# Performance work log

Hardware: AMD Instinct MI355X
Metric: run time of the kernel (lower is better)

Reference implementation:

```python
import jax, jax.numpy as jnp
import numpy as np

K = 3
BN_EPS = 1e-3


def setup_inputs() -> dict:
    key = jax.random.key(0)
    ks = jax.random.split(key, 13)
    B, N1, N2 = 8, 1024, 4096
    C1, C2, Cs = 256, 128, 64
    Ctot = C1 + C2 + Cs  # 448
    H = 256
    return {
        "points1": jax.random.normal(ks[0], (B, 3, N1), jnp.float32),
        "points2": jax.random.normal(ks[1], (B, 3, N2), jnp.float32),
        "features1": jax.random.normal(ks[2], (B, C1, N1), jnp.float32),
        "features2": jax.random.normal(ks[3], (B, C2, N2), jnp.float32),
        "skip_features": jax.random.normal(ks[4], (B, Cs, N2), jnp.float32),
        # 1x1 Conv2d weights are equivalent to dense matrices [out, in]
        "W1": jax.random.normal(ks[5], (H, Ctot), jnp.float32) * 0.05,
        "b1": jax.random.normal(ks[6], (H,), jnp.float32) * 0.05,
        "g1": 1.0 + jax.random.normal(ks[7], (H,), jnp.float32) * 0.05,
        "beta1": jax.random.normal(ks[8], (H,), jnp.float32) * 0.05,
        "W2": jax.random.normal(ks[9], (H, H), jnp.float32) * 0.05,
        "b2": jax.random.normal(ks[10], (H,), jnp.float32) * 0.05,
        "g2": 1.0 + jax.random.normal(ks[11], (H,), jnp.float32) * 0.05,
        "beta2": jax.random.normal(ks[12], (H,), jnp.float32) * 0.05,
    }


def _conv_bn_relu(x, W, b, g, beta):
    # x: [B, N, Cin]; 1x1 conv == dense matmul per point
    y = jnp.einsum("bnc,oc->bno", x, W) + b
    # BatchNorm2d in training mode: batch stats over (batch, spatial) per channel
    mu = jnp.mean(y, axis=(0, 1))
    var = jnp.mean(jnp.square(y - mu), axis=(0, 1))  # biased variance
    y = (y - mu) * jax.lax.rsqrt(var + BN_EPS) * g + beta
    return jax.nn.relu(y)


def reference(points1, points2, features1, features2, skip_features,
              W1, b1, g1, beta1, W2, b2, g2, beta2):
    p1 = jnp.swapaxes(points1, 1, 2)  # [B, N1, 3]
    p2 = jnp.swapaxes(points2, 1, 2)  # [B, N2, 3]
    # pairwise Euclidean distances [B, N2, N1]
    d2 = (jnp.sum(p2 * p2, -1, keepdims=True)
          + jnp.sum(p1 * p1, -1)[:, None, :]
          - 2.0 * jnp.einsum("bnd,bmd->bnm", p2, p1))
    dist = jnp.sqrt(jnp.maximum(d2, 0.0))
    # k smallest distances
    neg_top, ind = jax.lax.top_k(-dist, K)  # ind: [B, N2, K]
    dk = -neg_top
    inv = 1.0 / (dk + 1e-10)
    w = inv / jnp.sum(inv, -1, keepdims=True)  # [B, N2, K]
    f1 = jnp.swapaxes(features1, 1, 2)  # [B, N1, C1]
    gathered = jax.vmap(lambda f, i: f[i])(f1, ind)  # [B, N2, K, C1]
    new = jnp.einsum("bnkc,bnk->bnc", gathered, w)  # inverse-distance interp
    x = jnp.concatenate([new,
                         jnp.swapaxes(features2, 1, 2),
                         jnp.swapaxes(skip_features, 1, 2)], axis=-1)
    x = _conv_bn_relu(x, W1, b1, g1, beta1)
    x = _conv_bn_relu(x, W2, b2, g2, beta2)
    return jnp.swapaxes(x, 1, 2)  # [B, Cout, N2]
```

## Files before the change

### kernel.cpp

```cpp
#include <hip/hip_runtime.h>
#include <cstdint>
#include <cstddef>

#define B_    8
#define N1_   1024
#define N2_   4096
#define C1_   256
#define C2_   128
#define CS_   64
#define CT_   448
#define H_    256
#define ROWS_ (B_ * N2_)
#define XW_   192

typedef __attribute__((ext_vector_type(8))) short bf16x8;
typedef __attribute__((ext_vector_type(4))) float f32x4;
typedef unsigned short ushort_t;
typedef unsigned int   uint_t;

__device__ __forceinline__ ushort_t f2bf(float f) {
    uint_t u = __float_as_uint(f);
    u = (u + 0x7fffu + ((u >> 16) & 1u)) >> 16;
    return (ushort_t)u;
}
__device__ __forceinline__ float bf2f(ushort_t h) {
    return __uint_as_float(((uint_t)h) << 16);
}
__device__ __forceinline__ void glds16(const void* g, void* l) {
    __builtin_amdgcn_global_load_lds(
        (const __attribute__((address_space(1))) void*)g,
        (__attribute__((address_space(3))) void*)l, 16, 0, 0);
}

__device__ __forceinline__ void tile_decode(int d, int& m0, int& n0) {
    const int j = d >> 3;
    m0 = ((d & 7) * 32 + (j >> 2)) * 128;
    n0 = (j & 3) * 64;
}

__global__ __launch_bounds__(256) void fused_pre(
    const float* __restrict__ p1, const float* __restrict__ p2,
    int* __restrict__ ind, float* __restrict__ wout,
    const float* __restrict__ f1, const float* __restrict__ f2,
    const float* __restrict__ fs, const float* __restrict__ W1,
    const float* __restrict__ W2, ushort_t* __restrict__ f1t,
    ushort_t* __restrict__ x, ushort_t* __restrict__ W1b, ushort_t* __restrict__ W2b)
{
#pragma clang fp contract(off)
    __shared__ __align__(16) char smem[32000];
    const int t = threadIdx.x;
    const int bid = blockIdx.x;
    if (bid < 1024) {
        float4*   cand  = (float4*)(smem);
        float*    pvals = (float*)(smem + 16512);
        float*    thr   = (float*)(smem + 19584);
        ushort_t* lists = (ushort_t*)(smem + 19712);
        float*    pdd   = (float*)(smem + 25856);
        int*      pdi   = (int*)(smem + 28928);
        const int b  = bid >> 7;
        const int qb = (bid & 127) * 32;
        const float* pb1 = p1 + (size_t)b * 3 * N1_;
        for (int i = t; i < N1_; i += 256) {
            float X = pb1[i], Y = pb1[N1_ + i], Z = pb1[2 * N1_ + i];
            cand[i] = make_float4(X, Y, Z, (X * X + Y * Y) + Z * Z);
        }
        const int q = t & 31, split = t >> 5;
        const int n = qb + q;
        const float* pb2 = p2 + (size_t)b * 3 * N2_;
        const float ax = pb2[n], ay = pb2[N2_ + n], az = pb2[2 * N2_ + n];
        const float s2a = (ax * ax + ay * ay) + az * az;
        const float m2x = -2.0f * ax, m2y = -2.0f * ay, m2z = -2.0f * az;
        __syncthreads();
        const int ibeg = split * 128, iend = ibeg + 128;
        {
            float a0 = 3e38f, a1 = 3e38f, a2 = 3e38f;
            for (int i = ibeg; i < iend; ++i) {
                float4 c = cand[i];
                float fd = fmaf(c.x, m2x, fmaf(c.y, m2y, fmaf(c.z, m2z, s2a + c.w)));
                float o0 = a0, o1 = a1;
                a0 = fminf(o0, fd);
                a1 = __builtin_amdgcn_fmed3f(fd, o0, o1);
                a2 = __builtin_amdgcn_fmed3f(fd, o1, a2);
            }
            pvals[t * 3 + 0] = a0; pvals[t * 3 + 1] = a1; pvals[t * 3 + 2] = a2;
        }
        __syncthreads();
        if (t < 32) {
            float m0 = 3e38f, m1 = 3e38f, m2v = 3e38f;
#pragma unroll
            for (int g = 0; g < 8; ++g)
#pragma unroll
                for (int r = 0; r < 3; ++r) {
                    float v = pvals[(g * 32 + t) * 3 + r];
                    float o0 = m0, o1 = m1;
                    m0 = fminf(o0, v);
                    m1 = __builtin_amdgcn_fmed3f(v, o0, o1);
                    m2v = __builtin_amdgcn_fmed3f(v, o1, m2v);
                }
            thr[t] = m2v + 2e-3f;
        }
        __syncthreads();
        const float th = thr[q];
        ushort_t* mylist = lists + (q * 8 + split) * 12;
        int cnt = 0;
        for (int i = ibeg; i < iend; ++i) {
            float4 c = cand[i];
            float fd = fmaf(c.x, m2x, fmaf(c.y, m2y, fmaf(c.z, m2z, s2a + c.w)));
            if (fd <= th && cnt < 12) { mylist[cnt] = (ushort_t)i; cnt++; }
        }
        float e0 = 3e38f, e1 = 3e38f, e2 = 3e38f;
        int   j0 = 0, j1 = 0, j2 = 0;
        for (int k = 0; k < cnt; ++k) {
            const int i = mylist[k];
            float4 c = cand[i];
            float dot = (ax * c.x + ay * c.y) + az * c.z;
            float dd  = (s2a + c.w) - 2.0f * dot;
            float d   = sqrtf(fmaxf(dd, 0.0f));
            if (d < e0)      { e2 = e1; j2 = j1; e1 = e0; j1 = j0; e0 = d; j0 = i; }
            else if (d < e1) { e2 = e1; j2 = j1; e1 = d;  j1 = i; }
            else if (d < e2) { e2 = d;  j2 = i; }
        }
        pdd[(split * 32 + q) * 3 + 0] = e0; pdi[(split * 32 + q) * 3 + 0] = j0;
        pdd[(split * 32 + q) * 3 + 1] = e1; pdi[(split * 32 + q) * 3 + 1] = j1;
        pdd[(split * 32 + q) * 3 + 2] = e2; pdi[(split * 32 + q) * 3 + 2] = j2;
        __syncthreads();
        if (t < 32) {
            float f0 = 3e38f, f1v = 3e38f, f2v = 3e38f;
            int   k0 = 0, k1 = 0, k2 = 0;
#pragma unroll
            for (int g = 0; g < 8; ++g)
#pragma unroll
                for (int r = 0; r < 3; ++r) {
                    float d = pdd[(g * 32 + t) * 3 + r];
                    int   i = pdi[(g * 32 + t) * 3 + r];
                    if (d < f0)       { f2v = f1v; k2 = k1; f1v = f0; k1 = k0; f0 = d; k0 = i; }
                    else if (d < f1v) { f2v = f1v; k2 = k1; f1v = d;  k1 = i; }
                    else if (d < f2v) { f2v = d;  k2 = i; }
                }
            float inv0 = 1.0f / (f0 + 1e-10f);
            float inv1 = 1.0f / (f1v + 1e-10f);
            float inv2 = 1.0f / (f2v + 1e-10f);
            float s = (inv0 + inv1) + inv2;
            const size_t row = (size_t)b * N2_ + qb + t;
            wout[row * 3 + 0] = inv0 / s;
            wout[row * 3 + 1] = inv1 / s;
            wout[row * 3 + 2] = inv2 / s;
            ind[row * 3 + 0] = k0;
            ind[row * 3 + 1] = k1;
            ind[row * 3 + 2] = k2;
        }
    } else if (bid < 1536) {
        float (*tile)[65] = (float (*)[65])smem;
        const int bid2 = bid - 1024;
        const int b  = bid2 >> 6;
        const int ct = (bid2 >> 4) & 3;
        const int nt = bid2 & 15;
        const int c0 = ct * 64, n0 = nt * 64;
        const float* src = f1 + ((size_t)b * C1_ + c0) * N1_ + n0;
#pragma unroll
        for (int j = 0; j < 16; ++j) {
            int lin = j * 256 + t;
            int ci = lin >> 6, nj = lin & 63;
            tile[ci][nj] = src[(size_t)ci * N1_ + nj];
        }
        __syncthreads();
        ushort_t* dst = f1t + ((size_t)b * N1_ + n0) * C1_ + c0;
#pragma unroll
        for (int j = 0; j < 8; ++j) {
            int lin = j * 256 + t;
            int ni = lin >> 5, cjp = (lin & 31) * 2;
            uint_t u = (uint_t)f2bf(tile[cjp][ni]) | ((uint_t)f2bf(tile[cjp + 1][ni]) << 16);
            *(uint_t*)&dst[(size_t)ni * C1_ + cjp] = u;
        }
    } else if (bid < 3072) {
        float (*tile)[65] = (float (*)[65])smem;
        const int bid2 = bid - 1536;
        const int b   = bid2 / 192;
        const int rem = bid2 - b * 192;
        const int ct  = rem >> 6;
        const int nt  = rem & 63;
        const float* src;
        if (ct < 2) src = f2 + ((size_t)b * C2_ + ct * 64) * N2_;
        else        src = fs + (size_t)b * CS_ * N2_;
        const int coff = ct * 64;
        const int n0 = nt * 64;
#pragma unroll
        for (int j = 0; j < 16; ++j) {
            int lin = j * 256 + t;
            int ci = lin >> 6, nj = lin & 63;
            tile[ci][nj] = src[(size_t)ci * N2_ + n0 + nj];
        }
        __syncthreads();
#pragma unroll
        for (int j = 0; j < 8; ++j) {
            int lin = j * 256 + t;
            int ni = lin >> 5, cjp = (lin & 31) * 2;
            uint_t u = (uint_t)f2bf(tile[cjp][ni]) | ((uint_t)f2bf(tile[cjp + 1][ni]) << 16);
            *(uint_t*)&x[((size_t)b * N2_ + n0 + ni) * XW_ + coff + cjp] = u;
        }
    } else {
        const int i = (bid - 3072) * 256 + t;
        if (i < H_ * CT_) W1b[i] = f2bf(W1[i]);
        if (i < H_ * H_)  W2b[i] = f2bf(W2[i]);
    }
}

__global__ __launch_bounds__(512, 6) void gemm1_fused(
    const ushort_t* __restrict__ f1t, const int* __restrict__ ind,
    const float* __restrict__ wgt, const ushort_t* __restrict__ x2,
    const ushort_t* __restrict__ Bw, const float* __restrict__ bias,
    ushort_t* __restrict__ C, float* __restrict__ ssum, float* __restrict__ ssq)
{
    __shared__ __align__(16) ushort_t smem[20480];
    ushort_t* As = smem;
    ushort_t* Bs = smem + 4096;
    ushort_t* Cs = smem;
    const int t = threadIdx.x;
    const int m0 = blockIdx.x * 64;
    const int lane = t & 63;
    const int wv = t >> 6;
    const int wr = wv & 1;
    const int wc = wv >> 1;
    const int lm = lane & 15, lq = lane >> 4;
    const int lrow8  = lane >> 3;
    const int lchunk = (lane & 7) ^ lrow8;
    const int aswz = lm & 7;
    const ushort_t* gB = Bw + (size_t)(wv * 32 + lrow8) * CT_ + lchunk * 8;
    ushort_t* lB = Bs + wv * 2048;
    const ushort_t* gA = x2 + (size_t)(m0 + wv * 8 + lrow8) * XW_ + lchunk * 8;
    ushort_t* lA = As + wv * 512;
    const int arow = t >> 3;
    const int ac0  = t & 7;
    const size_t grow = (size_t)m0 + arow;
    const int bb_ = (int)(grow >> 12);
    const int* ip = ind + grow * 3;
    const float* wp = wgt + grow * 3;
    const ushort_t* fb = f1t + (size_t)bb_ * N1_ * C1_;
    const ushort_t* ga0 = fb + (size_t)ip[0] * C1_ + ac0 * 8;
    const ushort_t* ga1 = fb + (size_t)ip[1] * C1_ + ac0 * 8;
    const ushort_t* ga2 = fb + (size_t)ip[2] * C1_ + ac0 * 8;
    const float w0 = wp[0], w1 = wp[1], w2 = wp[2];
    ushort_t* awr = As + arow * 64;
    const int arsw = arow & 7;
    f32x4 acc[2][4];
#pragma unroll
    for (int i = 0; i < 2; ++i)
#pragma unroll
        for (int j = 0; j < 4; ++j)
            acc[i][j] = (f32x4){0.f, 0.f, 0.f, 0.f};

    for (int k0 = 0; k0 < CT_; k0 += 64) {
        __syncthreads();
        if (k0 < 256) {
            uint4 va = *(const uint4*)(ga0 + k0);
            uint4 vb = *(const uint4*)(ga1 + k0);
            uint4 vc = *(const uint4*)(ga2 + k0);
            const uint_t* pa = (const uint_t*)&va;
            const uint_t* pb = (const uint_t*)&vb;
            const uint_t* pc = (const uint_t*)&vc;
            uint_t o[4];
#pragma unroll
            for (int e = 0; e < 4; ++e) {
                float lo = w0 * bf2f((ushort_t)(pa[e] & 0xffff))
                         + w1 * bf2f((ushort_t)(pb[e] & 0xffff))
                         + w2 * bf2f((ushort_t)(pc[e] & 0xffff));
                float hi = w0 * bf2f((ushort_t)(pa[e] >> 16))
                         + w1 * bf2f((ushort_t)(pb[e] >> 16))
                         + w2 * bf2f((ushort_t)(pc[e] >> 16));
                o[e] = (uint_t)f2bf(lo) | ((uint_t)f2bf(hi) << 16);
            }
            *(uint4*)&awr[(ac0 ^ arsw) * 8] = *(uint4*)o;
        } else {
            glds16(gA + (k0 - 256), lA);
        }
#pragma unroll
        for (int g = 0; g < 4; ++g)
            glds16(gB + k0 + g * 8 * CT_, lB + g * 512);
        __syncthreads();
#pragma unroll
        for (int h = 0; h < 2; ++h) {
            bf16x8 af[2], bfr[4];
#pragma unroll
            for (int i = 0; i < 2; ++i)
                af[i] = *(const bf16x8*)&As[(wr * 32 + i * 16 + lm) * 64
                                            + (((h * 4 + lq) ^ aswz)) * 8];
#pragma unroll
            for (int j = 0; j < 4; ++j)
                bfr[j] = *(const bf16x8*)&Bs[(wc * 64 + j * 16 + lm) * 64
                                             + (((h * 4 + lq) ^ aswz)) * 8];
#pragma unroll
            for (int i = 0; i < 2; ++i)
#pragma unroll
                for (int j = 0; j < 4; ++j)
                    acc[i][j] = __builtin_amdgcn_mfma_f32_16x16x32_bf16(af[i], bfr[j], acc[i][j], 0, 0, 0);
        }
    }
    __syncthreads();
#pragma unroll
    for (int j = 0; j < 4; ++j) {
        const int gn = wc * 64 + j * 16 + lm;
        const float bb = bias[gn];
        float ps = 0.0f, pq = 0.0f;
#pragma unroll
        for (int i = 0; i < 2; ++i) {
            const int row_l = wr * 32 + i * 16 + lq * 4;
            f32x4 v = acc[i][j];
#pragma unroll
            for (int r = 0; r < 4; ++r) {
                float val = v[r] + bb;
                ps += val;
                pq += val * val;
                float vo = __shfl_xor(val, 1);
                uint_t packed = (lm & 1)
                    ? ((uint_t)f2bf(vo)  | ((uint_t)f2bf(val) << 16))
                    : ((uint_t)f2bf(val) | ((uint_t)f2bf(vo)  << 16));
                if ((lm & 1) == 0)
                    *(uint_t*)&Cs[(row_l + r) * 264 + (gn & ~1)] = packed;
            }
        }
        ps += __shfl_xor(ps, 16); pq += __shfl_xor(pq, 16);
        ps += __shfl_xor(ps, 32); pq += __shfl_xor(pq, 32);
        if (lane < 16) {
            atomicAdd(&ssum[gn], ps);
            atomicAdd(&ssq[gn], pq);
        }
    }
    __syncthreads();
    const int srow = t >> 5;
    const int scol = (t & 31) * 8;
#pragma unroll
    for (int rep = 0; rep < 4; ++rep) {
        const int row = srow + rep * 16;
        uint4 v = *(const uint4*)&Cs[row * 264 + scol];
        *(uint4*)(C + (size_t)(m0 + row) * H_ + scol) = v;
    }
}

__global__ __launch_bounds__(256, 4) void gemm2_fused(
    const ushort_t* __restrict__ A, const ushort_t* __restrict__ Bw,
    const float* __restrict__ bias,
    const float* __restrict__ s1, const float* __restrict__ q1,
    const float* __restrict__ g1, const float* __restrict__ be1,
    ushort_t* __restrict__ C, float* __restrict__ ssum, float* __restrict__ ssq)
{
    __shared__ __align__(16) ushort_t smem[15360];
    ushort_t* As0 = smem;
    ushort_t* As1 = smem + 5120;
    ushort_t* Bs  = smem + 10240;
    float*    sc  = (float*)(smem + 14336);
    float*    sh  = (float*)(smem + 14848);
    ushort_t* Cs  = smem;
    const int t = threadIdx.x;
    int m0, n0;
    tile_decode(blockIdx.x, m0, n0);
    const int lane = t & 63;
    const int wv = t >> 6;
    const int wrow = wv & 1, wcol = wv >> 1;
    const int lm = lane & 15, lq = lane >> 4;
    const int lrow8  = lane >> 3;
    const int lchunk = (lane & 7) ^ lrow8;
    const int aswz = lm & 7;
    const int arow = t >> 1, acol = (t & 1) * 32;
    {
        const float invN = 1.0f / (float)ROWS_;
        float mu  = s1[t] * invN;
        float var = q1[t] * invN - mu * mu;
        float s   = rsqrtf(var + 1e-3f) * g1[t];
        sc[t] = s;
        sh[t] = be1[t] - mu * s;
    }
    const ushort_t* gB = Bw + (size_t)(n0 + wv * 16 + lrow8) * H_ + lchunk * 8;
    ushort_t* lB = Bs + wv * 1024;
    const ushort_t* gA = A + (size_t)(m0 + arow) * H_ + acol;
    ushort_t* As_t = (t & 1) ? As1 : As0;
    f32x4 acc[4][2];
#pragma unroll
    for (int i = 0; i < 4; ++i)
#pragma unroll
        for (int j = 0; j < 2; ++j)
            acc[i][j] = (f32x4){0.f, 0.f, 0.f, 0.f};

    for (int k0 = 0; k0 < H_; k0 += 64) {
        uint4 av[4];
#pragma unroll
        for (int g = 0; g < 4; ++g)
            av[g] = *(const uint4*)(gA + k0 + g * 8);
        __syncthreads();
#pragma unroll
        for (int g = 0; g < 2; ++g)
            glds16(gB + k0 + g * 8 * H_, lB + g * 512);
#pragma unroll
        for (int g = 0; g < 4; ++g) {
            const uint_t* wsrc = (const uint_t*)&av[g];
            uint_t o[4];
#pragma unroll
            for (int e = 0; e < 4; ++e) {
                const int cb = k0 + acol + g * 8 + 2 * e;
                float lo = __uint_as_float(wsrc[e] << 16);
                float hi = __uint_as_float(wsrc[e] & 0xffff0000u);
                float r0 = fmaxf(fmaf(lo, sc[cb],     sh[cb]),     0.0f);
                float r1 = fmaxf(fmaf(hi, sc[cb + 1], sh[cb + 1]), 0.0f);
                o[e] = (uint_t)f2bf(r0) | ((uint_t)f2bf(r1) << 16);
            }
            *(uint4*)&As_t[arow * 40 + g * 8] = *(uint4*)o;
        }
        __syncthreads();
#pragma unroll
        for (int h = 0; h < 2; ++h) {
            const ushort_t* Ah = h ? As1 : As0;
            bf16x8 af[4], bfr[2];
#pragma unroll
            for (int i = 0; i < 4; ++i)
                af[i] = *(const bf16x8*)&Ah[(wrow * 64 + i * 16 + lm) * 40 + lq * 8];
#pragma unroll
            for (int j = 0; j < 2; ++j)
                bfr[j] = *(const bf16x8*)&Bs[(wcol * 32 + j * 16 + lm) * 64
                                             + (((h * 4 + lq) ^ aswz)) * 8];
#pragma unroll
            for (int i = 0; i < 4; ++i)
#pragma unroll
                for (int j = 0; j < 2; ++j)
                    acc[i][j] = __builtin_amdgcn_mfma_f32_16x16x32_bf16(af[i], bfr[j], acc[i][j], 0, 0, 0);
        }
    }
    __syncthreads();
#pragma unroll
    for (int j = 0; j < 2; ++j) {
        const int gn_l = wcol * 32 + j * 16 + lm;
        const int gn   = n0 + gn_l;
        const float bb = bias[gn];
        float ps = 0.0f, pq = 0.0f;
#pragma unroll
        for (int i = 0; i < 4; ++i) {
            const int row_l = wrow * 64 + i * 16 + lq * 4;
            f32x4 v = acc[i][j];
#pragma unroll
            for (int r = 0; r < 4; ++r) {
                float val = v[r] + bb;
                ps += val;
                pq += val * val;
                float vo = __shfl_xor(val, 1);
                uint_t packed = (lm & 1)
                    ? ((uint_t)f2bf(vo)  | ((uint_t)f2bf(val) << 16))
                    : ((uint_t)f2bf(val) | ((uint_t)f2bf(vo)  << 16));
                if ((lm & 1) == 0)
                    *(uint_t*)&Cs[(row_l + r) * 72 + (gn_l & ~1)] = packed;
            }
        }
        ps += __shfl_xor(ps, 16); pq += __shfl_xor(pq, 16);
        ps += __shfl_xor(ps, 32); pq += __shfl_xor(pq, 32);
        if (lane < 16) {
            atomicAdd(&ssum[gn], ps);
            atomicAdd(&ssq[gn], pq);
        }
    }
    __syncthreads();
    const int srow = t >> 3;
    const int scol = (t & 7) * 8;
#pragma unroll
    for (int rep = 0; rep < 4; ++rep) {
        const int row = srow + rep * 32;
        uint4 v = *(const uint4*)&Cs[row * 72 + scol];
        *(uint4*)(C + (size_t)(m0 + row) * H_ + n0 + scol) = v;
    }
}

__global__ __launch_bounds__(256) void bn_out_kernel(
    const ushort_t* __restrict__ y, const float* __restrict__ ssum, const float* __restrict__ ssq,
    const float* __restrict__ g, const float* __restrict__ beta, float* __restrict__ out)
{
    __shared__ float tile[64][65];
    __shared__ float sc[64], sh[64];
    const float invN = 1.0f / (float)ROWS_;
    const int bid = blockIdx.x;
    const int b  = bid >> 8;
    const int nt = (bid >> 2) & 63;
    const int ot = bid & 3;
    const int t = threadIdx.x;
    if (t < 64) {
        int c = ot * 64 + t;
        float mu  = ssum[c] * invN;
        float var = ssq[c] * invN - mu * mu;
        float s   = rsqrtf(var + 1e-3f) * g[c];
        sc[t] = s;
        sh[t] = beta[c] - mu * s;
    }
    __syncthreads();
    const int n0 = nt * 64, o0 = ot * 64;
    const ushort_t* yb = y + ((size_t)b * N2_ + n0) * H_ + o0;
#pragma unroll
    for (int j = 0; j < 8; ++j) {
        int lin = j * 256 + t;
        int nl = lin >> 5, cu = (lin & 31) * 2;
        uint_t u = *(const uint_t*)&yb[(size_t)nl * H_ + cu];
        tile[nl][cu]     = fmaxf(bf2f((ushort_t)(u & 0xffff)) * sc[cu]     + sh[cu],     0.0f);
        tile[nl][cu + 1] = fmaxf(bf2f((ushort_t)(u >> 16))    * sc[cu + 1] + sh[cu + 1], 0.0f);
    }
    __syncthreads();
    float* ob = out + ((size_t)b * H_ + o0) * N2_ + n0;
#pragma unroll
    for (int j = 0; j < 16; ++j) {
        int lin = j * 256 + t;
        int ol = lin >> 6, nl = lin & 63;
        ob[(size_t)ol * N2_ + nl] = tile[nl][ol];
    }
}

extern "C" void kernel_launch(void* const* d_in, const int* in_sizes, int n_in,
                              void* d_out, int out_size, void* d_ws, size_t ws_size,
                              hipStream_t stream)
{
    (void)in_sizes; (void)n_in; (void)out_size; (void)ws_size;
    const float* points1   = (const float*)d_in[0];
    const float* points2   = (const float*)d_in[1];
    const float* features1 = (const float*)d_in[2];
    const float* features2 = (const float*)d_in[3];
    const float* skipf     = (const float*)d_in[4];
    const float* W1  = (const float*)d_in[5];
    const float* b1  = (const float*)d_in[6];
    const float* g1  = (const float*)d_in[7];
    const float* be1 = (const float*)d_in[8];
    const float* W2  = (const float*)d_in[9];
    const float* b2  = (const float*)d_in[10];
    const float* g2  = (const float*)d_in[11];
    const float* be2 = (const float*)d_in[12];
    float* out = (float*)d_out;

    char* ws = (char*)d_ws;
    float*    s1  = (float*)(ws + 0);
    float*    q1  = (float*)(ws + 1024);
    float*    s2  = (float*)(ws + 2048);
    float*    q2  = (float*)(ws + 3072);
    int*      ind = (int*)(ws + 4096);
    float*    wgt = (float*)(ws + 397312);
    ushort_t* x   = (ushort_t*)(ws + 790528);
    ushort_t* y1b = (ushort_t*)(ws + 30150656);
    ushort_t* W1b = (ushort_t*)(ws + 63705088);
    ushort_t* W2b = (ushort_t*)(ws + 63934464);
    ushort_t* f1t = (ushort_t*)(ws + 64065536);
    ushort_t* y2b = x;

    hipMemsetAsync(ws, 0, 4096, stream);

    fused_pre<<<dim3(3520), dim3(256), 0, stream>>>(points1, points2, ind, wgt,
                                                    features1, features2, skipf,
                                                    W1, W2, f1t, x, W1b, W2b);

    gemm1_fused<<<dim3(ROWS_ / 64), dim3(512), 0, stream>>>(f1t, ind, wgt, x,
                                                            W1b, b1, y1b, s1, q1);
    gemm2_fused<<<dim3(ROWS_ / 128 * 4), dim3(256), 0, stream>>>(y1b, W2b, b2, s1, q1, g1, be1, y2b, s2, q2);
    bn_out_kernel<<<dim3(2048), dim3(256), 0, stream>>>(y2b, s2, q2, g2, be2, out);
}
```

Before: 204.3 us.

## Prefetch all interpolation gathers upfront into a full-width LDS A tile

The gemm1 kernel now issues all twelve feature-gather loads for the interpolated 256-channel part at the start, blends them, and stores the whole 64x256 A slab to LDS once. It no longer does one gather per K-step inside the main loop. The K loop is split into an interpolation phase that reads only B tiles and a second phase for the features2/skip columns. This is meant to expose more memory-level parallelism for the random gathers and shorten the per-iteration critical path. In exchange, LDS use grows to about 72KB and the occupancy hint drops from 6 to 4 blocks, which raises register pressure and lowers occupancy.

```diff
diff --git a/kernel.cpp b/kernel.cpp
--- a/kernel.cpp
+++ b/kernel.cpp
@@ -205,16 +205,17 @@
     }
 }
 
-__global__ __launch_bounds__(512, 6) void gemm1_fused(
+__global__ __launch_bounds__(512, 4) void gemm1_fused(
     const ushort_t* __restrict__ f1t, const int* __restrict__ ind,
     const float* __restrict__ wgt, const ushort_t* __restrict__ x2,
     const ushort_t* __restrict__ Bw, const float* __restrict__ bias,
     ushort_t* __restrict__ C, float* __restrict__ ssum, float* __restrict__ ssq)
 {
-    __shared__ __align__(16) ushort_t smem[20480];
-    ushort_t* As = smem;
-    ushort_t* Bs = smem + 4096;
-    ushort_t* Cs = smem;
+    __shared__ __align__(16) ushort_t smem[36864];
+    ushort_t* Abig   = smem;
+    ushort_t* Asmall = smem + 16384;
+    ushort_t* Bs     = smem + 20480;
+    ushort_t* Cs     = smem;
     const int t = threadIdx.x;
     const int m0 = blockIdx.x * 64;
     const int lane = t & 63;
@@ -228,36 +229,34 @@
     const ushort_t* gB = Bw + (size_t)(wv * 32 + lrow8) * CT_ + lchunk * 8;
     ushort_t* lB = Bs + wv * 2048;
     const ushort_t* gA = x2 + (size_t)(m0 + wv * 8 + lrow8) * XW_ + lchunk * 8;
-    ushort_t* lA = As + wv * 512;
-    const int arow = t >> 3;
-    const int ac0  = t & 7;
-    const size_t grow = (size_t)m0 + arow;
-    const int bb_ = (int)(grow >> 12);
-    const int* ip = ind + grow * 3;
-    const float* wp = wgt + grow * 3;
-    const ushort_t* fb = f1t + (size_t)bb_ * N1_ * C1_;
-    const ushort_t* ga0 = fb + (size_t)ip[0] * C1_ + ac0 * 8;
-    const ushort_t* ga1 = fb + (size_t)ip[1] * C1_ + ac0 * 8;
-    const ushort_t* ga2 = fb + (size_t)ip[2] * C1_ + ac0 * 8;
-    const float w0 = wp[0], w1 = wp[1], w2 = wp[2];
-    ushort_t* awr = As + arow * 64;
-    const int arsw = arow & 7;
-    f32x4 acc[2][4];
-#pragma unroll
-    for (int i = 0; i < 2; ++i)
-#pragma unroll
-        for (int j = 0; j < 4; ++j)
-            acc[i][j] = (f32x4){0.f, 0.f, 0.f, 0.f};
-
-    for (int k0 = 0; k0 < CT_; k0 += 64) {
-        __syncthreads();
-        if (k0 < 256) {
-            uint4 va = *(const uint4*)(ga0 + k0);
-            uint4 vb = *(const uint4*)(ga1 + k0);
-            uint4 vc = *(const uint4*)(ga2 + k0);
-            const uint_t* pa = (const uint_t*)&va;
-            const uint_t* pb = (const uint_t*)&vb;
-            const uint_t* pc = (const uint_t*)&vc;
+    ushort_t* lA = Asmall + wv * 512;
+
+    {
+        const int arow = t >> 3;
+        const int tc   = t & 7;
+        const size_t grow = (size_t)m0 + arow;
+        const int bb_ = (int)(grow >> 12);
+        const int* ip = ind + grow * 3;
+        const float* wp = wgt + grow * 3;
+        const ushort_t* fb = f1t + (size_t)bb_ * N1_ * C1_;
+        const ushort_t* ga0 = fb + (size_t)ip[0] * C1_ + tc * 8;
+        const ushort_t* ga1 = fb + (size_t)ip[1] * C1_ + tc * 8;
+        const ushort_t* ga2 = fb + (size_t)ip[2] * C1_ + tc * 8;
+        const float w0 = wp[0], w1 = wp[1], w2 = wp[2];
+        const int slot3 = tc ^ (arow & 7);
+        ushort_t* awr = Abig + arow * 256 + slot3 * 8;
+        uint4 va[4], vb[4], vc[4];
+#pragma unroll
+        for (int g = 0; g < 4; ++g) {
+            va[g] = *(const uint4*)(ga0 + g * 64);
+            vb[g] = *(const uint4*)(ga1 + g * 64);
+            vc[g] = *(const uint4*)(ga2 + g * 64);
+        }
+#pragma unroll
+        for (int g = 0; g < 4; ++g) {
+            const uint_t* pa = (const uint_t*)&va[g];
+            const uint_t* pb = (const uint_t*)&vb[g];
+            const uint_t* pc = (const uint_t*)&vc[g];
             uint_t o[4];
 #pragma unroll
             for (int e = 0; e < 4; ++e) {
@@ -269,10 +268,19 @@
                          + w2 * bf2f((ushort_t)(pc[e] >> 16));
                 o[e] = (uint_t)f2bf(lo) | ((uint_t)f2bf(hi) << 16);
             }
-            *(uint4*)&awr[(ac0 ^ arsw) * 8] = *(uint4*)o;
-        } else {
-            glds16(gA + (k0 - 256), lA);
-        }
+            *(uint4*)&awr[g * 64] = *(uint4*)o;
+        }
+    }
+
+    f32x4 acc[2][4];
+#pragma unroll
+    for (int i = 0; i < 2; ++i)
+#pragma unroll
+        for (int j = 0; j < 4; ++j)
+            acc[i][j] = (f32x4){0.f, 0.f, 0.f, 0.f};
+
+    for (int k0 = 0; k0 < 256; k0 += 64) {
+        __syncthreads();
 #pragma unroll
         for (int g = 0; g < 4; ++g)
             glds16(gB + k0 + g * 8 * CT_, lB + g * 512);
@@ -282,8 +290,8 @@
             bf16x8 af[2], bfr[4];
 #pragma unroll
             for (int i = 0; i < 2; ++i)
-                af[i] = *(const bf16x8*)&As[(wr * 32 + i * 16 + lm) * 64
-                                            + (((h * 4 + lq) ^ aswz)) * 8];
+                af[i] = *(const bf16x8*)&Abig[(wr * 32 + i * 16 + lm) * 256
+                                              + k0 + (((h * 4 + lq) ^ aswz)) * 8];
 #pragma unroll
             for (int j = 0; j < 4; ++j)
                 bfr[j] = *(const bf16x8*)&Bs[(wc * 64 + j * 16 + lm) * 64
@@ -295,6 +303,32 @@
                     acc[i][j] = __builtin_amdgcn_mfma_f32_16x16x32_bf16(af[i], bfr[j], acc[i][j], 0, 0, 0);
         }
     }
+    for (int k0 = 256; k0 < CT_; k0 += 64) {
+        __syncthreads();
+        glds16(gA + (k0 - 256), lA);
+#pragma unroll
+        for (int g = 0; g < 4; ++g)
+            glds16(gB + k0 + g * 8 * CT_, lB + g * 512);
+        __syncthreads();
+#pragma unroll
+        for (int h = 0; h < 2; ++h) {
+            bf16x8 af[2], bfr[4];
+#pragma unroll
+            for (int i = 0; i < 2; ++i)
+                af[i] = *(const bf16x8*)&Asmall[(wr * 32 + i * 16 + lm) * 64
+                                                + (((h * 4 + lq) ^ aswz)) * 8];
+#pragma unroll
+            for (int j = 0; j < 4; ++j)
+                bfr[j] = *(const bf16x8*)&Bs[(wc * 64 + j * 16 + lm) * 64
+                                             + (((h * 4 + lq) ^ aswz)) * 8];
+#pragma unroll
+            for (int i = 0; i < 2; ++i)
+#pragma unroll
+                for (int j = 0; j < 4; ++j)
+                    acc[i][j] = __builtin_amdgcn_mfma_f32_16x16x32_bf16(af[i], bfr[j], acc[i][j], 0, 0, 0);
+        }
+    }
+
     __syncthreads();
 #pragma unroll
     for (int j = 0; j < 4; ++j) {
```

Result: no change. 200.4 us (-1.9%).
